# Kernel optimization log

Measured on AMD Instinct MI355X. Metric: run time of the kernel, lower is better.

Reference implementation:

```python
import jax, jax.numpy as jnp
import numpy as np

NUM_ENT = 100000   # entity vocabulary
NUM_EDGES = 200000 # KB pairs processed per hop (max_act)
D = 768            # BERT hidden size
NSTEP = 3          # num hops
QLEN = 32          # question length


def setup_inputs() -> dict:
    key = jax.random.key(0)
    ks = jax.random.split(key, 18)
    rn = lambda k, s, scale=1.0: jax.random.normal(k, s, dtype=jnp.float32) * scale
    W = 0.02  # weight init scale
    return {
        "q_emb": rn(ks[0], (1, D)),
        "q_word_h": rn(ks[1], (1, QLEN, D)),
        "desc_emb": rn(ks[2], (NUM_EDGES, D)),
        "step_w1": rn(ks[3], (NSTEP, D, D), W),
        "step_b1": rn(ks[4], (NSTEP, D), W),
        "step_w2": rn(ks[5], (NSTEP, D, D), W),
        "step_b2": rn(ks[6], (NSTEP, D), W),
        "rel_w1": rn(ks[7], (D, 256), W),
        "rel_b1": rn(ks[8], (256,), W),
        "rel_w2": rn(ks[9], (256,), W),
        "rel_b2": rn(ks[10], (1,), W),
        "hop_w1": rn(ks[11], (D, 256), W),
        "hop_b1": rn(ks[12], (256,), W),
        "hop_w2": rn(ks[13], (256, NSTEP), W),
        "hop_b2": rn(ks[14], (NSTEP,), W),
        "kb_pair": jax.random.randint(ks[15], (NUM_EDGES, 2), 0, NUM_ENT, dtype=jnp.int32),
        "topic_ent_idxs": jax.random.randint(ks[16], (4,), 0, NUM_ENT, dtype=jnp.int32),
    }


def reference(q_emb, q_word_h, desc_emb, step_w1, step_b1, step_w2, step_b2,
              rel_w1, rel_b1, rel_w2, rel_b2, hop_w1, hop_b1, hop_w2, hop_b2,
              kb_pair, topic_ent_idxs):
    gelu = lambda x: jax.nn.gelu(x, approximate=False)  # torch nn.GELU default
    # topic entity one-hot init (idx_to_one_hot)
    last_e = jnp.zeros((NUM_ENT,), jnp.float32).at[topic_ent_idxs].set(1.0)
    sub, obj = kb_pair[:, 0], kb_pair[:, 1]
    ent_probs = []
    for t in range(NSTEP):
        # step encoder: Linear -> GELU -> Linear
        cq = gelu(q_emb @ step_w1[t] + step_b1[t]) @ step_w2[t] + step_b2[t]  # [1,D]
        # attention over question words
        q_logits = jnp.einsum('bd,bld->bl', cq, q_word_h)                      # [1,L]
        q_dist = jax.nn.softmax(q_logits, axis=1)
        ctx = jnp.einsum('bl,bld->bd', q_dist, q_word_h) + cq                  # [1,D]
        # relation classifier over edge descriptions: Linear -> GELU -> Linear
        h = gelu((ctx * desc_emb) @ rel_w1 + rel_b1)                           # [E,256]
        d_prob = jax.nn.sigmoid(h @ rel_w2 + rel_b2)                           # [E]
        # follow: gather subject scores, scatter-add to objects
        obj_p = last_e[sub] * d_prob
        last_e = jax.ops.segment_sum(obj_p, obj, num_segments=NUM_ENT)
        # clamp-style renormalization (detached divisor)
        z = jax.lax.stop_gradient(jnp.where(last_e > 1.0, last_e, 1.0))
        last_e = last_e / z
        ent_probs.append(last_e)
    hop_res = jnp.stack(ent_probs, 0)                                          # [T,N]
    hop_attn = jax.nn.softmax(gelu(q_emb @ hop_w1 + hop_b1) @ hop_w2 + hop_b2, axis=1)  # [1,T]
    return (hop_attn @ hop_res)[0]                                             # [N]
```

## Files before the change

### kernel.cpp

```cpp
#include <hip/hip_runtime.h>
#include <math.h>

#define NUM_ENT 100000
#define NUM_EDGES 200000
#define DIM 768
#define BM 96
#define KSTEPS 24
#define NC 16
#define DCH 48

typedef float f32x4 __attribute__((ext_vector_type(4)));
typedef __bf16 bf16x8 __attribute__((ext_vector_type(8)));
typedef unsigned short u16x4 __attribute__((ext_vector_type(4)));

#define WS_Y1    0
#define WS_CQ    2304
#define WS_HA    4704
#define WS_HOP1  4736
#define WS_CTX   4992
#define WS_B     7424
#define WS_DPROB 302336
#define WS_P1    302336
#define WS_P1H   339200
#define WS_P2    343296
#define WS_E     902336

__device__ __forceinline__ unsigned short f2bf(float f) {
    unsigned int x = __builtin_bit_cast(unsigned int, f);
    x = x + 0x7fffu + ((x >> 16) & 1u);
    return (unsigned short)(x >> 16);
}

__device__ __forceinline__ float gelu_f(float x) {
    float z = 0.70710678118654752f * x;
    float s = fabsf(z);
    float t = 1.f / (1.f + 0.3275911f * s);
    float p = t * (0.254829592f + t * (-0.284496736f + t * (1.421413741f +
              t * (-1.453152027f + t * 1.061405429f))));
    float e = __expf(-s * s);
    float erfa = copysignf(1.f - p * e, z);
    return 0.5f * x * (1.f + erfa);
}

__device__ __forceinline__ void gload16(const void* g, void* l) {
    __builtin_amdgcn_global_load_lds(
        (const __attribute__((address_space(1))) void*)g,
        (__attribute__((address_space(3))) void*)l, 16, 0, 0);
}

__global__ void k1a(const float* __restrict__ q, const float* __restrict__ sw1,
                    const float* __restrict__ hw1, float* __restrict__ ws) {
    int b = blockIdx.x, tid = threadIdx.x;
    if (b < 48) {
        int t = b >> 4, c = b & 15;
        const float* w = sw1 + (size_t)t * DIM * DIM + (size_t)c * DCH * DIM;
        float a0 = 0.f, a1 = 0.f, a2 = 0.f;
        for (int d = 0; d < DCH; ++d) {
            float qv = q[c * DCH + d];
            const float* wr = w + (size_t)d * DIM;
            a0 += qv * wr[tid]; a1 += qv * wr[tid + 256]; a2 += qv * wr[tid + 512];
        }
        float* p = ws + WS_P1 + (size_t)b * DIM;
        p[tid] = a0; p[tid + 256] = a1; p[tid + 512] = a2;
    } else {
        int c = b - 48;
        const float* w = hw1 + (size_t)c * DCH * 256;
        float a0 = 0.f;
        for (int d = 0; d < DCH; ++d) a0 += q[c * DCH + d] * w[(size_t)d * 256 + tid];
        ws[WS_P1H + c * 256 + tid] = a0;
    }
}

__global__ void k1b(const float* __restrict__ sb1, const float* __restrict__ hb1,
                    float* __restrict__ ws) {
    int o = blockIdx.x * 256 + threadIdx.x;
    if (o < 2304) {
        int t = o / DIM, j = o % DIM;
        float s = sb1[o];
        for (int c = 0; c < NC; ++c) s += ws[WS_P1 + (size_t)(t * 16 + c) * DIM + j];
        ws[WS_Y1 + o] = gelu_f(s);
    } else if (o < 2560) {
        int j = o - 2304;
        float s = hb1[j];
        for (int c = 0; c < NC; ++c) s += ws[WS_P1H + c * 256 + j];
        ws[WS_HOP1 + j] = gelu_f(s);
    }
}

__global__ void k2a(const float* __restrict__ sw2, float* __restrict__ ws) {
    int b = blockIdx.x, tid = threadIdx.x;
    int t = b >> 4, c = b & 15;
    const float* w = sw2 + (size_t)t * DIM * DIM + (size_t)c * DCH * DIM;
    const float* y = ws + WS_Y1 + t * DIM + c * DCH;
    float a0 = 0.f, a1 = 0.f, a2 = 0.f;
    for (int d = 0; d < DCH; ++d) {
        float yv = y[d];
        const float* wr = w + (size_t)d * DIM;
        a0 += yv * wr[tid]; a1 += yv * wr[tid + 256]; a2 += yv * wr[tid + 512];
    }
    float* p = ws + WS_P2 + (size_t)b * DIM;
    p[tid] = a0; p[tid + 256] = a1; p[tid + 512] = a2;
}

__global__ void k2b(const float* __restrict__ sb2, float* __restrict__ ws) {
    int o = blockIdx.x * 256 + threadIdx.x;
    int t = o / DIM, j = o % DIM;
    float s = sb2[o];
    for (int c = 0; c < NC; ++c) s += ws[WS_P2 + (size_t)(t * 16 + c) * DIM + j];
    ws[WS_CQ + o] = s;
}

__global__ void k345(const float* __restrict__ qwh, const float* __restrict__ hw2,
                     const float* __restrict__ hb2, float* __restrict__ ws) {
    __shared__ float qlog[96];
    int tid = threadIdx.x;
    int w = tid >> 6, lane = tid & 63;
    for (int s = 0; s < 6; ++s) {
        int p = w * 6 + s;
        int t = p >> 5, l = p & 31;
        const float* c = ws + WS_CQ + t * DIM;
        const float* qw = qwh + l * DIM;
        float acc = 0.f;
        for (int i = lane; i < DIM; i += 64) acc += c[i] * qw[i];
        for (int m = 32; m; m >>= 1) acc += __shfl_xor(acc, m);
        if (lane == 0) qlog[p] = acc;
    }
    __syncthreads();
    if (tid < 64) {
        for (int t = 0; t < 3; ++t) {
            float v = (lane < 32) ? qlog[t * 32 + lane] : -1e30f;
            float mx = v;
            for (int m = 1; m < 32; m <<= 1) mx = fmaxf(mx, __shfl_xor(mx, m, 32));
            float e = (lane < 32) ? __expf(v - mx) : 0.f;
            float s = e;
            for (int m = 1; m < 32; m <<= 1) s += __shfl_xor(s, m, 32);
            if (lane < 32) qlog[t * 32 + lane] = e / s;
        }
        float lg = 0.f;
        if (lane < 3) {
            for (int s = 0; s < 256; ++s) lg += ws[WS_HOP1 + s] * hw2[s * 3 + lane];
            lg += hb2[lane];
        }
        float l0 = __shfl(lg, 0), l1 = __shfl(lg, 1), l2 = __shfl(lg, 2);
        if (lane == 0) {
            float mx = fmaxf(l0, fmaxf(l1, l2));
            float e0 = __expf(l0 - mx), e1 = __expf(l1 - mx), e2 = __expf(l2 - mx);
            float s = e0 + e1 + e2;
            ws[WS_HA + 0] = e0 / s; ws[WS_HA + 1] = e1 / s; ws[WS_HA + 2] = e2 / s;
        }
    }
    __syncthreads();
    for (int o = tid; o < 2304; o += 1024) {
        int t = o / DIM, d = o % DIM;
        float acc = ws[WS_CQ + o];
        const float* qd = qlog + t * 32;
        for (int l = 0; l < 32; ++l) acc += qd[l] * qwh[l * DIM + d];
        ws[WS_CTX + o] = acc;
    }
}

__global__ void k6_bmat(const float* __restrict__ rw1, float* __restrict__ ws) {
    int g = blockIdx.x * 256 + threadIdx.x;
    int lane = g & 63, f = g >> 6;
    int ks = f / 48, r = f % 48;
    int t = r >> 4, cf = r & 15;
    int k0 = ks * 32 + (lane >> 4) * 8;
    int col = cf * 16 + (lane & 15);
    const float* ctx = ws + WS_CTX + t * DIM;
    union { unsigned short u[8]; bf16x8 v; } pk;
    #pragma unroll
    for (int j = 0; j < 8; ++j) {
        float v = ctx[k0 + j] * rw1[(size_t)(k0 + j) * 256 + col];
        pk.u[j] = f2bf(v);
    }
    *(bf16x8*)((unsigned short*)(ws + WS_B) + (size_t)g * 8) = pk.v;
}

__global__ __launch_bounds__(768, 3)
void k7_gemm(const float* __restrict__ desc, const float* __restrict__ rb1,
             const float* __restrict__ rw2, const float* __restrict__ rb2,
             float* __restrict__ ws) {
    extern __shared__ char lds[];
    unsigned short* bB = (unsigned short*)lds;
    unsigned short* aB = (unsigned short*)(lds + 98304);
    float* part = (float*)(lds + 110592);

    const unsigned short* bmat = (const unsigned short*)(ws + WS_B);
    float* dprob = ws + WS_DPROB;
    int tid = threadIdx.x;
    int blk = blockIdx.x;
    int wid = tid >> 6, lane = tid & 63;
    int t = wid >> 2, cg = wid & 3;
    int fbase = t * 16 + cg * 4;

    int arow = tid >> 3, aq = tid & 7;
    int rowg = blk * BM + arow;
    if (rowg > NUM_EDGES - 1) rowg = NUM_EDGES - 1;
    const float* asrc = desc + (size_t)rowg * DIM + aq * 4;
    int arf = arow >> 4, alr = arow & 15;
    int awoff = arf * 512 + (aq >> 1) * 128 + alr * 8 + (aq & 1) * 4;

    const char* bsrc0 = (const char*)bmat + wid * 4096 + lane * 16;
    char* bdst0 = (char*)bB + wid * 4096;

    f32x4 acc[6][4];
    #pragma unroll
    for (int rf = 0; rf < 6; ++rf)
        #pragma unroll
        for (int i = 0; i < 4; ++i) acc[rf][i] = f32x4{0.f, 0.f, 0.f, 0.f};

    {
        float4 av = *(const float4*)asrc;
        #pragma unroll
        for (int j = 0; j < 4; ++j) gload16(bsrc0 + j * 1024, bdst0 + j * 1024);
        u16x4 pk;
        pk.x = f2bf(av.x); pk.y = f2bf(av.y); pk.z = f2bf(av.z); pk.w = f2bf(av.w);
        *(u16x4*)&aB[awoff] = pk;
    }
    asm volatile("s_waitcnt lgkmcnt(0)" ::: "memory");
    __builtin_amdgcn_s_barrier();

    #pragma unroll 1
    for (int ks = 0; ks < KSTEPS; ++ks) {
        int cur = ks & 1, nxt = cur ^ 1;
        float4 av;
        if (ks < KSTEPS - 1) {
            av = *(const float4*)(asrc + (ks + 1) * 32);
            const char* bs = bsrc0 + (size_t)(ks + 1) * 49152;
            char* bd = bdst0 + nxt * 49152;
            #pragma unroll
            for (int j = 0; j < 4; ++j) gload16(bs + j * 1024, bd + j * 1024);
            asm volatile("s_waitcnt vmcnt(5)" ::: "memory");
        } else {
            asm volatile("s_waitcnt vmcnt(0)" ::: "memory");
        }
        __builtin_amdgcn_sched_barrier(0);

        const unsigned short* bb = bB + cur * 24576 + fbase * 512 + lane * 8;
        bf16x8 bfr[4];
        #pragma unroll
        for (int i = 0; i < 4; ++i) bfr[i] = *(const bf16x8*)(bb + i * 512);
        const unsigned short* ab = aB + cur * 3072 + lane * 8;

        __builtin_amdgcn_s_setprio(1);
        #pragma unroll
        for (int rf = 0; rf < 6; ++rf) {
            bf16x8 a = *(const bf16x8*)(ab + rf * 512);
            #pragma unroll
            for (int i = 0; i < 4; ++i)
                acc[rf][i] = __builtin_amdgcn_mfma_f32_16x16x32_bf16(a, bfr[i], acc[rf][i], 0, 0, 0);
        }
        __builtin_amdgcn_s_setprio(0);

        if (ks < KSTEPS - 1) {
            u16x4 pk;
            pk.x = f2bf(av.x); pk.y = f2bf(av.y); pk.z = f2bf(av.z); pk.w = f2bf(av.w);
            *(u16x4*)&aB[nxt * 3072 + awoff] = pk;
        }
        asm volatile("s_waitcnt lgkmcnt(0)" ::: "memory");
        __builtin_amdgcn_s_barrier();
    }

    int col16 = lane & 15, quart = lane >> 4;
    float b1v[4], w2v[4];
    #pragma unroll
    for (int i = 0; i < 4; ++i) {
        int c = cg * 64 + i * 16 + col16;
        b1v[i] = rb1[c]; w2v[i] = rw2[c];
    }
    #pragma unroll
    for (int rf = 0; rf < 6; ++rf) {
        #pragma unroll
        for (int r = 0; r < 4; ++r) {
            float s = 0.f;
            #pragma unroll
            for (int i = 0; i < 4; ++i)
                s += gelu_f(acc[rf][i][r] + b1v[i]) * w2v[i];
            #pragma unroll
            for (int m = 1; m < 16; m <<= 1) s += __shfl_xor(s, m);
            if (col16 == 0) part[wid * 96 + rf * 16 + quart * 4 + r] = s;
        }
    }
    __syncthreads();
    if (tid < 288) {
        int tt = tid / 96, row = tid % 96;
        float v = part[(tt * 4 + 0) * 96 + row] + part[(tt * 4 + 1) * 96 + row]
                + part[(tt * 4 + 2) * 96 + row] + part[(tt * 4 + 3) * 96 + row] + rb2[0];
        float p = 1.f / (1.f + __expf(-v));
        int rg = blk * BM + row;
        if (rg < NUM_EDGES) dprob[(size_t)tt * NUM_EDGES + rg] = p;
    }
}

__global__ void kzero(float* __restrict__ ws) {
    int i = blockIdx.x * 256 + threadIdx.x;
    if (i < 3 * NUM_ENT) ws[WS_E + NUM_ENT + i] = 0.f;
}

__global__ void k9_scatter(const int* __restrict__ kb, const int* __restrict__ topics,
                           float* __restrict__ ws, int t) {
    int e = blockIdx.x * 256 + threadIdx.x;
    if (e >= NUM_EDGES) return;
    int sub = kb[2 * e], obj = kb[2 * e + 1];
    float g;
    if (t == 0) {
        g = (sub == topics[0] || sub == topics[1] || sub == topics[2] || sub == topics[3]) ? 1.f : 0.f;
    } else {
        float v = ws[WS_E + (size_t)t * NUM_ENT + sub];
        g = v / fmaxf(v, 1.f);
    }
    float p = g * ws[WS_DPROB + (size_t)t * NUM_EDGES + e];
    if (p != 0.f) atomicAdd(&ws[WS_E + (size_t)(t + 1) * NUM_ENT + obj], p);
}

__global__ void kout(const float* __restrict__ ws, float* __restrict__ out) {
    int i = blockIdx.x * 256 + threadIdx.x;
    if (i >= NUM_ENT) return;
    float v1 = ws[WS_E + 1 * NUM_ENT + i]; v1 /= fmaxf(v1, 1.f);
    float v2 = ws[WS_E + 2 * NUM_ENT + i]; v2 /= fmaxf(v2, 1.f);
    float v3 = ws[WS_E + 3 * NUM_ENT + i]; v3 /= fmaxf(v3, 1.f);
    out[i] = ws[WS_HA + 0] * v1 + ws[WS_HA + 1] * v2 + ws[WS_HA + 2] * v3;
}

extern "C" void kernel_launch(void* const* d_in, const int* in_sizes, int n_in,
                              void* d_out, int out_size, void* d_ws, size_t ws_size,
                              hipStream_t stream) {
    const float* q_emb   = (const float*)d_in[0];
    const float* qwh     = (const float*)d_in[1];
    const float* desc    = (const float*)d_in[2];
    const float* sw1     = (const float*)d_in[3];
    const float* sb1     = (const float*)d_in[4];
    const float* sw2     = (const float*)d_in[5];
    const float* sb2     = (const float*)d_in[6];
    const float* rw1     = (const float*)d_in[7];
    const float* rb1     = (const float*)d_in[8];
    const float* rw2     = (const float*)d_in[9];
    const float* rb2     = (const float*)d_in[10];
    const float* hw1     = (const float*)d_in[11];
    const float* hb1     = (const float*)d_in[12];
    const float* hw2     = (const float*)d_in[13];
    const float* hb2     = (const float*)d_in[14];
    const int*   kb      = (const int*)d_in[15];
    const int*   topics  = (const int*)d_in[16];
    float* ws  = (float*)d_ws;
    float* out = (float*)d_out;

    int nblk7 = (NUM_EDGES + BM - 1) / BM;

    kzero<<<(3 * NUM_ENT + 255) / 256, 256, 0, stream>>>(ws);
    k1a<<<64, 256, 0, stream>>>(q_emb, sw1, hw1, ws);
    k1b<<<10, 256, 0, stream>>>(sb1, hb1, ws);
    k2a<<<48, 256, 0, stream>>>(sw2, ws);
    k2b<<<9, 256, 0, stream>>>(sb2, ws);
    k345<<<1, 1024, 0, stream>>>(qwh, hw2, hb2, ws);
    k6_bmat<<<288, 256, 0, stream>>>(rw1, ws);
    k7_gemm<<<nblk7, 768, 115200, stream>>>(desc, rb1, rw2, rb2, ws);
    for (int t = 0; t < 3; ++t)
        k9_scatter<<<(NUM_EDGES + 255) / 256, 256, 0, stream>>>(kb, topics, ws, t);
    kout<<<(NUM_ENT + 255) / 256, 256, 0, stream>>>(ws, out);
}
```

Baseline: 541.6 us.

## Restructure relation GEMM: stage whole A tile in LDS, stream B from registers

The relation-classifier GEMM now loads and converts the block's entire 64-row desc tile (all of K) into LDS once up front. B fragments are read directly from global memory into registers with a two-stage register double buffer, replacing the per-k-step LDS double buffering and barriers. The row tile shrinks from 96 to 64 rows so it divides the edge count exactly, which removes the bounds checks. This removes per-step barriers and B LDS traffic, but exposes the full desc load latency before any compute starts and makes B reads hit global/L2 from every block.

```diff
diff --git a/kernel.cpp b/kernel.cpp
--- a/kernel.cpp
+++ b/kernel.cpp
@@ -4,14 +4,13 @@
 #define NUM_ENT 100000
 #define NUM_EDGES 200000
 #define DIM 768
-#define BM 96
+#define BM 64
 #define KSTEPS 24
 #define NC 16
 #define DCH 48
 
 typedef float f32x4 __attribute__((ext_vector_type(4)));
 typedef __bf16 bf16x8 __attribute__((ext_vector_type(8)));
-typedef unsigned short u16x4 __attribute__((ext_vector_type(4)));
 
 #define WS_Y1    0
 #define WS_CQ    2304
@@ -40,12 +39,6 @@
     float e = __expf(-s * s);
     float erfa = copysignf(1.f - p * e, z);
     return 0.5f * x * (1.f + erfa);
-}
-
-__device__ __forceinline__ void gload16(const void* g, void* l) {
-    __builtin_amdgcn_global_load_lds(
-        (const __attribute__((address_space(1))) void*)g,
-        (__attribute__((address_space(3))) void*)l, 16, 0, 0);
 }
 
 __global__ void k1a(const float* __restrict__ q, const float* __restrict__ sw1,
@@ -176,89 +169,90 @@
     *(bf16x8*)((unsigned short*)(ws + WS_B) + (size_t)g * 8) = pk.v;
 }
 
+#define MFMA4(A, B0, B1, B2, B3, RF)                                               \
+    acc[RF][0] = __builtin_amdgcn_mfma_f32_16x16x32_bf16(A, B0, acc[RF][0], 0,0,0); \
+    acc[RF][1] = __builtin_amdgcn_mfma_f32_16x16x32_bf16(A, B1, acc[RF][1], 0,0,0); \
+    acc[RF][2] = __builtin_amdgcn_mfma_f32_16x16x32_bf16(A, B2, acc[RF][2], 0,0,0); \
+    acc[RF][3] = __builtin_amdgcn_mfma_f32_16x16x32_bf16(A, B3, acc[RF][3], 0,0,0);
+
 __global__ __launch_bounds__(768, 3)
 void k7_gemm(const float* __restrict__ desc, const float* __restrict__ rb1,
              const float* __restrict__ rw2, const float* __restrict__ rb2,
              float* __restrict__ ws) {
     extern __shared__ char lds[];
-    unsigned short* bB = (unsigned short*)lds;
-    unsigned short* aB = (unsigned short*)(lds + 98304);
-    float* part = (float*)(lds + 110592);
+    unsigned short* aLds = (unsigned short*)lds;
+    float* part = (float*)(lds + 98304);
 
     const unsigned short* bmat = (const unsigned short*)(ws + WS_B);
     float* dprob = ws + WS_DPROB;
-    int tid = threadIdx.x;
-    int blk = blockIdx.x;
+    int tid = threadIdx.x, blk = blockIdx.x;
     int wid = tid >> 6, lane = tid & 63;
     int t = wid >> 2, cg = wid & 3;
-    int fbase = t * 16 + cg * 4;
-
-    int arow = tid >> 3, aq = tid & 7;
-    int rowg = blk * BM + arow;
-    if (rowg > NUM_EDGES - 1) rowg = NUM_EDGES - 1;
-    const float* asrc = desc + (size_t)rowg * DIM + aq * 4;
-    int arf = arow >> 4, alr = arow & 15;
-    int awoff = arf * 512 + (aq >> 1) * 128 + alr * 8 + (aq & 1) * 4;
-
-    const char* bsrc0 = (const char*)bmat + wid * 4096 + lane * 16;
-    char* bdst0 = (char*)bB + wid * 4096;
-
-    f32x4 acc[6][4];
-    #pragma unroll
-    for (int rf = 0; rf < 6; ++rf)
+    int fbase = (t << 4) + (cg << 2);
+
+    const unsigned short* bp = bmat + ((size_t)fbase << 9) + lane * 8;
+    bf16x8 b0_0 = *(const bf16x8*)(bp);
+    bf16x8 b0_1 = *(const bf16x8*)(bp + 512);
+    bf16x8 b0_2 = *(const bf16x8*)(bp + 1024);
+    bf16x8 b0_3 = *(const bf16x8*)(bp + 1536);
+    bp += 48 * 512;
+
+    #pragma unroll
+    for (int i = 0; i < 8; ++i) {
+        int gf = i * 768 + tid;
+        int l = gf & 63, f = gf >> 6;
+        int ks = f >> 2, rf = f & 3;
+        int row = rf * 16 + (l & 15);
+        int kb = ks * 32 + (l >> 4) * 8;
+        const float* src = desc + (size_t)(blk * BM + row) * DIM + kb;
+        float4 v0 = *(const float4*)src;
+        float4 v1 = *(const float4*)(src + 4);
+        bf16x8 pk;
+        pk[0] = (__bf16)v0.x; pk[1] = (__bf16)v0.y; pk[2] = (__bf16)v0.z; pk[3] = (__bf16)v0.w;
+        pk[4] = (__bf16)v1.x; pk[5] = (__bf16)v1.y; pk[6] = (__bf16)v1.z; pk[7] = (__bf16)v1.w;
+        *(bf16x8*)(aLds + (size_t)f * 512 + l * 8) = pk;
+    }
+    __syncthreads();
+
+    f32x4 acc[4][4];
+    #pragma unroll
+    for (int rf = 0; rf < 4; ++rf)
         #pragma unroll
         for (int i = 0; i < 4; ++i) acc[rf][i] = f32x4{0.f, 0.f, 0.f, 0.f};
 
-    {
-        float4 av = *(const float4*)asrc;
-        #pragma unroll
-        for (int j = 0; j < 4; ++j) gload16(bsrc0 + j * 1024, bdst0 + j * 1024);
-        u16x4 pk;
-        pk.x = f2bf(av.x); pk.y = f2bf(av.y); pk.z = f2bf(av.z); pk.w = f2bf(av.w);
-        *(u16x4*)&aB[awoff] = pk;
-    }
-    asm volatile("s_waitcnt lgkmcnt(0)" ::: "memory");
-    __builtin_amdgcn_s_barrier();
+    const unsigned short* ab0 = aLds + lane * 8;
+    bf16x8 b1_0, b1_1, b1_2, b1_3;
 
     #pragma unroll 1
-    for (int ks = 0; ks < KSTEPS; ++ks) {
-        int cur = ks & 1, nxt = cur ^ 1;
-        float4 av;
-        if (ks < KSTEPS - 1) {
-            av = *(const float4*)(asrc + (ks + 1) * 32);
-            const char* bs = bsrc0 + (size_t)(ks + 1) * 49152;
-            char* bd = bdst0 + nxt * 49152;
-            #pragma unroll
-            for (int j = 0; j < 4; ++j) gload16(bs + j * 1024, bd + j * 1024);
-            asm volatile("s_waitcnt vmcnt(5)" ::: "memory");
-        } else {
-            asm volatile("s_waitcnt vmcnt(0)" ::: "memory");
-        }
-        __builtin_amdgcn_sched_barrier(0);
-
-        const unsigned short* bb = bB + cur * 24576 + fbase * 512 + lane * 8;
-        bf16x8 bfr[4];
-        #pragma unroll
-        for (int i = 0; i < 4; ++i) bfr[i] = *(const bf16x8*)(bb + i * 512);
-        const unsigned short* ab = aB + cur * 3072 + lane * 8;
-
-        __builtin_amdgcn_s_setprio(1);
-        #pragma unroll
-        for (int rf = 0; rf < 6; ++rf) {
-            bf16x8 a = *(const bf16x8*)(ab + rf * 512);
-            #pragma unroll
-            for (int i = 0; i < 4; ++i)
-                acc[rf][i] = __builtin_amdgcn_mfma_f32_16x16x32_bf16(a, bfr[i], acc[rf][i], 0, 0, 0);
-        }
-        __builtin_amdgcn_s_setprio(0);
-
-        if (ks < KSTEPS - 1) {
-            u16x4 pk;
-            pk.x = f2bf(av.x); pk.y = f2bf(av.y); pk.z = f2bf(av.z); pk.w = f2bf(av.w);
-            *(u16x4*)&aB[nxt * 3072 + awoff] = pk;
-        }
-        asm volatile("s_waitcnt lgkmcnt(0)" ::: "memory");
-        __builtin_amdgcn_s_barrier();
+    for (int ks = 0; ks < KSTEPS; ks += 2) {
+        b1_0 = *(const bf16x8*)(bp);
+        b1_1 = *(const bf16x8*)(bp + 512);
+        b1_2 = *(const bf16x8*)(bp + 1024);
+        b1_3 = *(const bf16x8*)(bp + 1536);
+        bp += 48 * 512;
+        {
+            const unsigned short* ab = ab0 + (size_t)ks * 2048;
+            bf16x8 a;
+            a = *(const bf16x8*)(ab);          MFMA4(a, b0_0, b0_1, b0_2, b0_3, 0)
+            a = *(const bf16x8*)(ab + 512);    MFMA4(a, b0_0, b0_1, b0_2, b0_3, 1)
+            a = *(const bf16x8*)(ab + 1024);   MFMA4(a, b0_0, b0_1, b0_2, b0_3, 2)
+            a = *(const bf16x8*)(ab + 1536);   MFMA4(a, b0_0, b0_1, b0_2, b0_3, 3)
+        }
+        if (ks + 2 < KSTEPS) {
+            b0_0 = *(const bf16x8*)(bp);
+            b0_1 = *(const bf16x8*)(bp + 512);
+            b0_2 = *(const bf16x8*)(bp + 1024);
+            b0_3 = *(const bf16x8*)(bp + 1536);
+            bp += 48 * 512;
+        }
+        {
+            const unsigned short* ab = ab0 + (size_t)ks * 2048 + 2048;
+            bf16x8 a;
+            a = *(const bf16x8*)(ab);          MFMA4(a, b1_0, b1_1, b1_2, b1_3, 0)
+            a = *(const bf16x8*)(ab + 512);    MFMA4(a, b1_0, b1_1, b1_2, b1_3, 1)
+            a = *(const bf16x8*)(ab + 1024);   MFMA4(a, b1_0, b1_1, b1_2, b1_3, 2)
+            a = *(const bf16x8*)(ab + 1536);   MFMA4(a, b1_0, b1_1, b1_2, b1_3, 3)
+        }
     }
 
     int col16 = lane & 15, quart = lane >> 4;
@@ -269,7 +263,7 @@
         b1v[i] = rb1[c]; w2v[i] = rw2[c];
     }
     #pragma unroll
-    for (int rf = 0; rf < 6; ++rf) {
+    for (int rf = 0; rf < 4; ++rf) {
         #pragma unroll
         for (int r = 0; r < 4; ++r) {
             float s = 0.f;
@@ -278,17 +272,16 @@
                 s += gelu_f(acc[rf][i][r] + b1v[i]) * w2v[i];
             #pragma unroll
             for (int m = 1; m < 16; m <<= 1) s += __shfl_xor(s, m);
-            if (col16 == 0) part[wid * 96 + rf * 16 + quart * 4 + r] = s;
+            if (col16 == 0) part[wid * 64 + rf * 16 + quart * 4 + r] = s;
         }
     }
     __syncthreads();
-    if (tid < 288) {
-        int tt = tid / 96, row = tid % 96;
-        float v = part[(tt * 4 + 0) * 96 + row] + part[(tt * 4 + 1) * 96 + row]
-                + part[(tt * 4 + 2) * 96 + row] + part[(tt * 4 + 3) * 96 + row] + rb2[0];
+    if (tid < 192) {
+        int tt = tid >> 6, row = tid & 63;
+        float v = part[(tt * 4 + 0) * 64 + row] + part[(tt * 4 + 1) * 64 + row]
+                + part[(tt * 4 + 2) * 64 + row] + part[(tt * 4 + 3) * 64 + row] + rb2[0];
         float p = 1.f / (1.f + __expf(-v));
-        int rg = blk * BM + row;
-        if (rg < NUM_EDGES) dprob[(size_t)tt * NUM_EDGES + rg] = p;
+        dprob[(size_t)tt * NUM_EDGES + blk * BM + row] = p;
     }
 }
 
@@ -345,7 +338,7 @@
     float* ws  = (float*)d_ws;
     float* out = (float*)d_out;
 
-    int nblk7 = (NUM_EDGES + BM - 1) / BM;
+    int nblk7 = NUM_EDGES / BM;
 
     kzero<<<(3 * NUM_ENT + 255) / 256, 256, 0, stream>>>(ws);
     k1a<<<64, 256, 0, stream>>>(q_emb, sw1, hw1, ws);
@@ -354,7 +347,7 @@
     k2b<<<9, 256, 0, stream>>>(sb2, ws);
     k345<<<1, 1024, 0, stream>>>(qwh, hw2, hb2, ws);
     k6_bmat<<<288, 256, 0, stream>>>(rw1, ws);
-    k7_gemm<<<nblk7, 768, 115200, stream>>>(desc, rb1, rw2, rb2, ws);
+    k7_gemm<<<nblk7, 768, 101376, stream>>>(desc, rb1, rw2, rb2, ws);
     for (int t = 0; t < 3; ++t)
         k9_scatter<<<(NUM_EDGES + 255) / 256, 256, 0, stream>>>(kb, topics, ws, t);
     kout<<<(NUM_ENT + 255) / 256, 256, 0, stream>>>(ws, out);
```

Measured after the change: 463.5 us. 1.17x faster.
